# Performance work log

Measured on AMD Instinct MI355X. Metric: run time of the kernel, lower is better.

Reference implementation:

```python
import jax, jax.numpy as jnp
import numpy as np

N_NODES = 50000


def _gcn_conv(x, W, b, src, dst, n):
    # GCNConv (PyG semantics): x' = D^-1/2 (A + I) D^-1/2 (x W) + b
    h = x @ W  # [N, out]
    loop = jnp.arange(n, dtype=src.dtype)
    s = jnp.concatenate([src, loop])  # self-loops appended
    d = jnp.concatenate([dst, loop])
    deg = jax.ops.segment_sum(jnp.ones_like(d, dtype=h.dtype), d, num_segments=n)
    dinv = jnp.where(deg > 0, jax.lax.rsqrt(deg), 0.0)
    norm = dinv[s] * dinv[d]  # [E+N]
    msgs = norm[:, None] * h[s]  # gather: [E+N, out]
    out = jax.ops.segment_sum(msgs, d, num_segments=n)  # scatter-add
    return out + b


def setup_inputs() -> dict:
    key = jax.random.key(0)
    ks = jax.random.split(key, 6)
    n, din, dh, dout, e = N_NODES, 64, 64, 16, 1600000
    x = jax.random.normal(ks[0], (n, din), dtype=jnp.float32)
    edge_index = jax.random.randint(ks[1], (2, e), 0, n, dtype=jnp.int64)
    W1 = jax.random.normal(ks[2], (din, dh), dtype=jnp.float32) / np.sqrt(din)
    b1 = jnp.zeros((dh,), dtype=jnp.float32)
    W2 = jax.random.normal(ks[3], (dh, dout), dtype=jnp.float32) / np.sqrt(dh)
    b2 = jnp.zeros((dout,), dtype=jnp.float32)
    return {"x": x, "edge_index": edge_index, "W1": W1, "b1": b1, "W2": W2, "b2": b2}


def reference(x, edge_index, W1, b1, W2, b2):
    n = x.shape[0]
    src, dst = edge_index[0], edge_index[1]
    h = _gcn_conv(x, W1, b1, src, dst, n)
    h = jax.nn.relu(h)
    h = _gcn_conv(h, W2, b2, src, dst, n)
    return jax.nn.log_softmax(h, axis=1)
```

## Files before the change

### kernel.cpp

```cpp
#include <hip/hip_runtime.h>
#include <hip/hip_bf16.h>
#include <math.h>

#define BSHIFT 6
#define BNODES 64
#define MAXB 1024
#define SORTCAP 4096

__device__ __forceinline__ bool detect_f64(const void* edges, long long nn) {
    const long long* e64 = (const long long*)edges;
    bool ok = true;
#pragma unroll
    for (int i = 0; i < 8; ++i) {
        long long v = e64[i];
        ok = ok && (v >= 0 && v < nn);
    }
    return ok;
}

__device__ __forceinline__ float bf16lo(unsigned int u) {
    return __uint_as_float(u << 16);
}
__device__ __forceinline__ float bf16hi(unsigned int u) {
    return __uint_as_float(u & 0xFFFF0000u);
}
__device__ __forceinline__ float bf16dec(unsigned short u) {
    return __uint_as_float(((unsigned int)u) << 16);
}
__device__ __forceinline__ unsigned short bf16enc(float f) {
    __hip_bfloat16 h = __float2bfloat16(f);
    return *reinterpret_cast<unsigned short*>(&h);
}

__global__ __launch_bounds__(512) void k_hist(const void* edges, long long nn,
                                              long long E, long long epb,
                                              int nbuckets, int nblk, int* partial) {
    __shared__ int cnt[MAXB];
    int t = threadIdx.x;
    int i = blockIdx.x;
    for (int b = t; b < nbuckets; b += 512) cnt[b] = 0;
    __syncthreads();
    bool f64 = detect_f64(edges, nn);
    long long e0 = (long long)i * epb;
    long long e1 = e0 + epb; if (e1 > E) e1 = E;
    for (long long e = e0 + t; e < e1; e += 512) {
        int d = f64 ? (int)((const long long*)edges)[E + e] : ((const int*)edges)[E + e];
        atomicAdd(&cnt[d >> BSHIFT], 1);
    }
    __syncthreads();
    for (int b = t; b < nbuckets; b += 512) partial[b * nblk + i] = cnt[b];
}

__global__ __launch_bounds__(256) void k_scanB(int* partial, int nblk, int* totals) {
    __shared__ int tmp[256];
    int b = blockIdx.x, t = threadIdx.x;
    int v = (t < nblk) ? partial[b * nblk + t] : 0;
    tmp[t] = v;
    __syncthreads();
    for (int off = 1; off < 256; off <<= 1) {
        int a = (t >= off) ? tmp[t - off] : 0;
        __syncthreads();
        tmp[t] += a;
        __syncthreads();
    }
    if (t < nblk) partial[b * nblk + t] = tmp[t] - v;
    if (t == 255) totals[b] = tmp[255];
}

__global__ __launch_bounds__(1024) void k_scan(const int* __restrict__ totals, int nbuckets,
                                               int* base) {
    __shared__ int tmp[MAXB];
    int t = threadIdx.x;
    int v = (t < nbuckets) ? totals[t] : 0;
    tmp[t] = v;
    __syncthreads();
    for (int off = 1; off < MAXB; off <<= 1) {
        int a = (t >= off) ? tmp[t - off] : 0;
        __syncthreads();
        tmp[t] += a;
        __syncthreads();
    }
    if (t < nbuckets) base[t] = tmp[t] - v;
}

__global__ __launch_bounds__(512) void k_place(const void* edges, long long nn,
                                               long long E, long long epb,
                                               int nbuckets, int nblk,
                                               const int* __restrict__ base,
                                               const int* __restrict__ partial,
                                               unsigned int* keys) {
    __shared__ int cur[MAXB];
    int t = threadIdx.x;
    int i = blockIdx.x;
    for (int b = t; b < nbuckets; b += 512) cur[b] = base[b] + partial[b * nblk + i];
    __syncthreads();
    bool f64 = detect_f64(edges, nn);
    long long e0 = (long long)i * epb;
    long long e1 = e0 + epb; if (e1 > E) e1 = E;
    for (long long e = e0 + t; e < e1; e += 512) {
        int s, d;
        if (f64) {
            const long long* ee = (const long long*)edges;
            s = (int)ee[e]; d = (int)ee[E + e];
        } else {
            const int* ee = (const int*)edges;
            s = ee[e]; d = ee[E + e];
        }
        int pos = atomicAdd(&cur[d >> BSHIFT], 1);
        keys[pos] = (unsigned int)s | ((unsigned int)(d & (BNODES - 1)) << 17);
    }
}

__global__ __launch_bounds__(256) void k_sortdeg(unsigned int* keys,
                                                 const int* __restrict__ base,
                                                 const int* __restrict__ totals,
                                                 int* rowstart, int* counts,
                                                 float* dinv, int n,
                                                 unsigned int* scratch) {
    __shared__ unsigned int kbuf[SORTCAP];
    __shared__ int hist[BNODES];
    __shared__ int cur[BNODES];
    int t = threadIdx.x;
    int bk = blockIdx.x;
    int st = base[bk], c = totals[bk];
    if (t < BNODES) hist[t] = 0;
    __syncthreads();
    bool fits = (c <= SORTCAP);
    if (fits) {
        for (int i = t; i < c; i += 256) {
            unsigned int k = keys[st + i];
            kbuf[i] = k;
            atomicAdd(&hist[k >> 17], 1);
        }
    } else {
        for (int i = t; i < c; i += 256) {
            unsigned int k = keys[st + i];
            scratch[st + i] = k;
            atomicAdd(&hist[k >> 17], 1);
        }
    }
    __syncthreads();
    if (t < 64) {
        int v = hist[t];
        int incl = v;
        for (int o = 1; o < 64; o <<= 1) {
            int other = __shfl_up(incl, o, 64);
            if (t >= o) incl += other;
        }
        int ex = incl - v;
        cur[t] = ex;
        int node = bk * BNODES + t;
        if (node < n) {
            rowstart[node] = st + ex;
            counts[node] = v;
            dinv[node] = rsqrtf((float)v + 1.0f);
        }
    }
    __syncthreads();
    if (fits) {
        for (int i = t; i < c; i += 256) {
            unsigned int k = kbuf[i];
            int pos = atomicAdd(&cur[k >> 17], 1);
            keys[st + pos] = k & 0x1FFFFu;
        }
    } else {
        for (int i = t; i < c; i += 256) {
            unsigned int k = scratch[st + i];
            int pos = atomicAdd(&cur[k >> 17], 1);
            keys[st + pos] = k & 0x1FFFFu;
        }
    }
}

__global__ __launch_bounds__(256) void k_gemm1(const float* __restrict__ x,
                                               const float* __restrict__ W,
                                               const float* __restrict__ dinv,
                                               unsigned short* __restrict__ h) {
    __shared__ float Ws[64][64];
    __shared__ float xs[16][64];
    int t = threadIdx.x;
    for (int i = t; i < 64 * 64; i += 256) Ws[i >> 6][i & 63] = W[i];
    long long row0 = (long long)blockIdx.x * 16;
    ((float4*)xs)[t] = ((const float4*)(x + row0 * 64))[t];
    __syncthreads();
    int r = t >> 4, c0 = (t & 15) * 4;
    float4 acc = {0.f, 0.f, 0.f, 0.f};
#pragma unroll
    for (int k = 0; k < 64; ++k) {
        float xv = xs[r][k];
        float4 wv = *((const float4*)&Ws[k][c0]);
        acc.x += xv * wv.x; acc.y += xv * wv.y;
        acc.z += xv * wv.z; acc.w += xv * wv.w;
    }
    float di = dinv[row0 + r];
    ushort4 pk;
    pk.x = bf16enc(di * acc.x);
    pk.y = bf16enc(di * acc.y);
    pk.z = bf16enc(di * acc.z);
    pk.w = bf16enc(di * acc.w);
    *((ushort4*)(h + (row0 + r) * 64 + c0)) = pk;
}

__global__ __launch_bounds__(256) void k_gemm2(const unsigned short* __restrict__ h,
                                               const float* __restrict__ W,
                                               const float* __restrict__ dinv,
                                               unsigned short* __restrict__ h2) {
    __shared__ float Ws[64 * 16];
    __shared__ float xs[16][64];
    int t = threadIdx.x;
    for (int i = t; i < 64 * 16; i += 256) Ws[i] = W[i];
    long long row0 = (long long)blockIdx.x * 16;
    ushort4 u4 = ((const ushort4*)(h + row0 * 64))[t];
    int lr = t >> 4, lc = (t & 15) * 4;
    xs[lr][lc + 0] = bf16dec(u4.x);
    xs[lr][lc + 1] = bf16dec(u4.y);
    xs[lr][lc + 2] = bf16dec(u4.z);
    xs[lr][lc + 3] = bf16dec(u4.w);
    __syncthreads();
    int r = t >> 4, c = t & 15;
    float acc = 0.f;
#pragma unroll
    for (int k = 0; k < 64; ++k) acc += xs[r][k] * Ws[k * 16 + c];
    h2[(row0 + r) * 16 + c] = bf16enc(dinv[row0 + r] * acc);
}

__global__ __launch_bounds__(256) void k_agg64(const int* __restrict__ rowstart,
                                               const int* __restrict__ counts,
                                               const unsigned int* __restrict__ srcs,
                                               const unsigned int* __restrict__ hb2,
                                               const float* __restrict__ dinv,
                                               const float* __restrict__ b,
                                               unsigned short* __restrict__ out, int n) {
    int d = (blockIdx.x * 256 + threadIdx.x) >> 6;
    if (d >= n) return;
    int lane = threadIdx.x & 63;
    int half = lane >> 5;
    int fl = lane & 31;
    float ax = 0.f, ay = 0.f;
    if (half == 0) {
        unsigned int u = hb2[(long long)d * 32 + fl];
        ax = bf16lo(u); ay = bf16hi(u);
    }
    int start = rowstart[d];
    int cnt = counts[d];
    int k = 0;
    for (; k + 8 <= cnt; k += 8) {
        unsigned int s0 = srcs[start + k + half];
        unsigned int s1 = srcs[start + k + 2 + half];
        unsigned int s2 = srcs[start + k + 4 + half];
        unsigned int s3 = srcs[start + k + 6 + half];
        unsigned int u0 = hb2[(long long)s0 * 32 + fl];
        unsigned int u1 = hb2[(long long)s1 * 32 + fl];
        unsigned int u2 = hb2[(long long)s2 * 32 + fl];
        unsigned int u3 = hb2[(long long)s3 * 32 + fl];
        ax += bf16lo(u0); ay += bf16hi(u0);
        ax += bf16lo(u1); ay += bf16hi(u1);
        ax += bf16lo(u2); ay += bf16hi(u2);
        ax += bf16lo(u3); ay += bf16hi(u3);
    }
    for (; k < cnt; k += 2) {
        int idx = k + half;
        unsigned int u0 = 0;
        if (idx < cnt) u0 = hb2[(long long)srcs[start + idx] * 32 + fl];
        ax += bf16lo(u0); ay += bf16hi(u0);
    }
    ax += __shfl_xor(ax, 32);
    ay += __shfl_xor(ay, 32);
    float di = dinv[d];
    float2 bb = ((const float2*)b)[fl];
    float ox = fmaxf(di * ax + bb.x, 0.f);
    float oy = fmaxf(di * ay + bb.y, 0.f);
    if (half == 0) {
        unsigned int pk = (unsigned int)bf16enc(ox) | ((unsigned int)bf16enc(oy) << 16);
        ((unsigned int*)(out + (long long)d * 64))[fl] = pk;
    }
}

__global__ __launch_bounds__(256) void k_agg16(const int* __restrict__ rowstart,
                                               const int* __restrict__ counts,
                                               const unsigned int* __restrict__ srcs,
                                               const unsigned short* __restrict__ hb,
                                               const float* __restrict__ dinv,
                                               const float* __restrict__ b,
                                               float* __restrict__ out, int n) {
    int g = (blockIdx.x * 256 + threadIdx.x) >> 4;
    if (g >= n) return;
    int f = threadIdx.x & 15;
    long long rb = (long long)g * 16;
    float acc = bf16dec(hb[rb + f]);
    int start = rowstart[g];
    int cnt = counts[g];
    int k = 0;
    for (; k + 8 <= cnt; k += 8) {
        unsigned int s0 = srcs[start + k];
        unsigned int s1 = srcs[start + k + 1];
        unsigned int s2 = srcs[start + k + 2];
        unsigned int s3 = srcs[start + k + 3];
        unsigned int s4 = srcs[start + k + 4];
        unsigned int s5 = srcs[start + k + 5];
        unsigned int s6 = srcs[start + k + 6];
        unsigned int s7 = srcs[start + k + 7];
        unsigned short u0 = hb[(long long)s0 * 16 + f];
        unsigned short u1 = hb[(long long)s1 * 16 + f];
        unsigned short u2 = hb[(long long)s2 * 16 + f];
        unsigned short u3 = hb[(long long)s3 * 16 + f];
        unsigned short u4 = hb[(long long)s4 * 16 + f];
        unsigned short u5 = hb[(long long)s5 * 16 + f];
        unsigned short u6 = hb[(long long)s6 * 16 + f];
        unsigned short u7 = hb[(long long)s7 * 16 + f];
        acc += bf16dec(u0); acc += bf16dec(u1); acc += bf16dec(u2); acc += bf16dec(u3);
        acc += bf16dec(u4); acc += bf16dec(u5); acc += bf16dec(u6); acc += bf16dec(u7);
    }
    for (; k < cnt; ++k) acc += bf16dec(hb[(long long)srcs[start + k] * 16 + f]);
    float v = dinv[g] * acc + b[f];
    float m = v;
#pragma unroll
    for (int o = 8; o >= 1; o >>= 1) m = fmaxf(m, __shfl_xor(m, o, 16));
    float ex = __expf(v - m);
#pragma unroll
    for (int o = 8; o >= 1; o >>= 1) ex += __shfl_xor(ex, o, 16);
    out[rb + f] = (v - m) - __logf(ex);
}

extern "C" void kernel_launch(void* const* d_in, const int* in_sizes, int n_in,
                              void* d_out, int out_size, void* d_ws, size_t ws_size,
                              hipStream_t stream) {
    const float* x  = (const float*)d_in[0];
    const void*  ei = d_in[1];
    const float* W1 = (const float*)d_in[2];
    const float* b1 = (const float*)d_in[3];
    const float* W2 = (const float*)d_in[4];
    const float* b2 = (const float*)d_in[5];

    long long dh  = in_sizes[3];
    long long din = in_sizes[2] / dh;
    long long n   = in_sizes[0] / din;
    long long E   = (long long)in_sizes[1] / 2;
    int nbuckets  = (int)((n + BNODES - 1) >> BSHIFT);

    long long epb = 8192;
    while ((E + epb - 1) / epb > 256) epb <<= 1;
    int nblk = (int)((E + epb - 1) / epb);

    char* ws = (char*)d_ws;
    auto alloc = [&](size_t bytes) { void* p = ws; ws += (bytes + 255) & ~255ULL; return p; };
    int*   totals   = (int*)alloc(nbuckets * 4);
    int*   base     = (int*)alloc(nbuckets * 4);
    int*   rowstart = (int*)alloc(n * 4);
    int*   counts   = (int*)alloc(n * 4);
    float* dinv     = (float*)alloc(n * 4);
    int*   partial  = (int*)alloc((size_t)nbuckets * nblk * 4);
    unsigned int* keys = (unsigned int*)alloc(E * 4);
    unsigned short* h1b  = (unsigned short*)alloc(n * 64 * 2);
    unsigned short* out1 = (unsigned short*)alloc(n * 64 * 2);
    unsigned short* h2b  = (unsigned short*)alloc(n * 16 * 2);
    unsigned int* sort_scratch = (unsigned int*)out1;

    float* out = (float*)d_out;

    k_hist<<<nblk, 512, 0, stream>>>(ei, n, E, epb, nbuckets, nblk, partial);
    k_scanB<<<nbuckets, 256, 0, stream>>>(partial, nblk, totals);
    k_scan<<<1, 1024, 0, stream>>>(totals, nbuckets, base);
    k_place<<<nblk, 512, 0, stream>>>(ei, n, E, epb, nbuckets, nblk, base, partial, keys);
    k_sortdeg<<<nbuckets, 256, 0, stream>>>(keys, base, totals, rowstart, counts,
                                            dinv, (int)n, sort_scratch);

    k_gemm1<<<(int)(n / 16), 256, 0, stream>>>(x, W1, dinv, h1b);
    k_agg64<<<(int)((n * 64 + 255) / 256), 256, 0, stream>>>(
        rowstart, counts, keys, (const unsigned int*)h1b, dinv, b1, out1, (int)n);

    k_gemm2<<<(int)(n / 16), 256, 0, stream>>>(out1, W2, dinv, h2b);
    k_agg16<<<(int)((n * 16 + 255) / 256), 256, 0, stream>>>(
        rowstart, counts, keys, h2b, dinv, b2, out, (int)n);
}
```

Before: 123.7 us.

## Vectorize aggregation gathers and fuse global bucket scan into last scanB block

The aggregation kernels now have each lane load 16-byte (layer 1) or 8-byte (layer 2) chunks of a neighbor's bf16 row, so several edges are processed in parallel per wavefront and then reduced with shuffles. The log-softmax epilogue works on four values per lane. The separate single-block bucket scan kernel is removed: the last k_scanB block, chosen by an atomic ticket, scans the totals, at the cost of a memset and a threadfence. This aims to cut the number of memory transactions per gather and one kernel launch, in exchange for more shuffle reductions.

```diff
diff --git a/kernel.cpp b/kernel.cpp
--- a/kernel.cpp
+++ b/kernel.cpp
@@ -51,8 +51,10 @@
     for (int b = t; b < nbuckets; b += 512) partial[b * nblk + i] = cnt[b];
 }
 
-__global__ __launch_bounds__(256) void k_scanB(int* partial, int nblk, int* totals) {
+__global__ __launch_bounds__(256) void k_scanB(int* partial, int nblk, int nbuckets,
+                                               int* totals, int* base, int* ticket) {
     __shared__ int tmp[256];
+    __shared__ int lastflag;
     int b = blockIdx.x, t = threadIdx.x;
     int v = (t < nblk) ? partial[b * nblk + t] : 0;
     tmp[t] = v;
@@ -64,23 +66,34 @@
         __syncthreads();
     }
     if (t < nblk) partial[b * nblk + t] = tmp[t] - v;
-    if (t == 255) totals[b] = tmp[255];
-}
-
-__global__ __launch_bounds__(1024) void k_scan(const int* __restrict__ totals, int nbuckets,
-                                               int* base) {
-    __shared__ int tmp[MAXB];
-    int t = threadIdx.x;
-    int v = (t < nbuckets) ? totals[t] : 0;
-    tmp[t] = v;
-    __syncthreads();
-    for (int off = 1; off < MAXB; off <<= 1) {
+    if (t == 255) {
+        totals[b] = tmp[255];
+        __threadfence();
+        int r = atomicAdd(ticket, 1);
+        lastflag = (r == (int)gridDim.x - 1);
+    }
+    __syncthreads();
+    if (!lastflag) return;
+    int i0 = t * 4;
+    int x0 = (i0 + 0 < nbuckets) ? atomicAdd(&totals[i0 + 0], 0) : 0;
+    int x1 = (i0 + 1 < nbuckets) ? atomicAdd(&totals[i0 + 1], 0) : 0;
+    int x2 = (i0 + 2 < nbuckets) ? atomicAdd(&totals[i0 + 2], 0) : 0;
+    int x3 = (i0 + 3 < nbuckets) ? atomicAdd(&totals[i0 + 3], 0) : 0;
+    int s4 = x0 + x1 + x2 + x3;
+    __syncthreads();
+    tmp[t] = s4;
+    __syncthreads();
+    for (int off = 1; off < 256; off <<= 1) {
         int a = (t >= off) ? tmp[t - off] : 0;
         __syncthreads();
         tmp[t] += a;
         __syncthreads();
     }
-    if (t < nbuckets) base[t] = tmp[t] - v;
+    int ex = tmp[t] - s4;
+    if (i0 + 0 < nbuckets) base[i0 + 0] = ex;
+    if (i0 + 1 < nbuckets) base[i0 + 1] = ex + x0;
+    if (i0 + 2 < nbuckets) base[i0 + 2] = ex + x0 + x1;
+    if (i0 + 3 < nbuckets) base[i0 + 3] = ex + x0 + x1 + x2;
 }
 
 __global__ __launch_bounds__(512) void k_place(const void* edges, long long nn,
@@ -224,102 +237,140 @@
     h2[(row0 + r) * 16 + c] = bf16enc(dinv[row0 + r] * acc);
 }
 
+#define ACC8(u) do { \
+    a0 += bf16lo((u).x); a1 += bf16hi((u).x); \
+    a2 += bf16lo((u).y); a3 += bf16hi((u).y); \
+    a4 += bf16lo((u).z); a5 += bf16hi((u).z); \
+    a6 += bf16lo((u).w); a7 += bf16hi((u).w); } while (0)
+
 __global__ __launch_bounds__(256) void k_agg64(const int* __restrict__ rowstart,
                                                const int* __restrict__ counts,
                                                const unsigned int* __restrict__ srcs,
-                                               const unsigned int* __restrict__ hb2,
+                                               const uint4* __restrict__ hb8,
                                                const float* __restrict__ dinv,
                                                const float* __restrict__ b,
                                                unsigned short* __restrict__ out, int n) {
     int d = (blockIdx.x * 256 + threadIdx.x) >> 6;
     if (d >= n) return;
     int lane = threadIdx.x & 63;
-    int half = lane >> 5;
-    int fl = lane & 31;
-    float ax = 0.f, ay = 0.f;
-    if (half == 0) {
-        unsigned int u = hb2[(long long)d * 32 + fl];
-        ax = bf16lo(u); ay = bf16hi(u);
+    int g8 = lane >> 3;
+    int fq = lane & 7;
+    float a0 = 0.f, a1 = 0.f, a2 = 0.f, a3 = 0.f;
+    float a4 = 0.f, a5 = 0.f, a6 = 0.f, a7 = 0.f;
+    if (g8 == 0) {
+        uint4 u = hb8[(long long)d * 8 + fq];
+        ACC8(u);
     }
     int start = rowstart[d];
     int cnt = counts[d];
     int k = 0;
+    for (; k + 16 <= cnt; k += 16) {
+        unsigned int s0 = srcs[start + k + g8];
+        unsigned int s1 = srcs[start + k + 8 + g8];
+        uint4 u0 = hb8[(long long)s0 * 8 + fq];
+        uint4 u1 = hb8[(long long)s1 * 8 + fq];
+        ACC8(u0);
+        ACC8(u1);
+    }
     for (; k + 8 <= cnt; k += 8) {
-        unsigned int s0 = srcs[start + k + half];
-        unsigned int s1 = srcs[start + k + 2 + half];
-        unsigned int s2 = srcs[start + k + 4 + half];
-        unsigned int s3 = srcs[start + k + 6 + half];
-        unsigned int u0 = hb2[(long long)s0 * 32 + fl];
-        unsigned int u1 = hb2[(long long)s1 * 32 + fl];
-        unsigned int u2 = hb2[(long long)s2 * 32 + fl];
-        unsigned int u3 = hb2[(long long)s3 * 32 + fl];
-        ax += bf16lo(u0); ay += bf16hi(u0);
-        ax += bf16lo(u1); ay += bf16hi(u1);
-        ax += bf16lo(u2); ay += bf16hi(u2);
-        ax += bf16lo(u3); ay += bf16hi(u3);
-    }
-    for (; k < cnt; k += 2) {
-        int idx = k + half;
-        unsigned int u0 = 0;
-        if (idx < cnt) u0 = hb2[(long long)srcs[start + idx] * 32 + fl];
-        ax += bf16lo(u0); ay += bf16hi(u0);
-    }
-    ax += __shfl_xor(ax, 32);
-    ay += __shfl_xor(ay, 32);
-    float di = dinv[d];
-    float2 bb = ((const float2*)b)[fl];
-    float ox = fmaxf(di * ax + bb.x, 0.f);
-    float oy = fmaxf(di * ay + bb.y, 0.f);
-    if (half == 0) {
-        unsigned int pk = (unsigned int)bf16enc(ox) | ((unsigned int)bf16enc(oy) << 16);
-        ((unsigned int*)(out + (long long)d * 64))[fl] = pk;
+        unsigned int s0 = srcs[start + k + g8];
+        uint4 u0 = hb8[(long long)s0 * 8 + fq];
+        ACC8(u0);
+    }
+    if (k + g8 < cnt) {
+        unsigned int s0 = srcs[start + k + g8];
+        uint4 u0 = hb8[(long long)s0 * 8 + fq];
+        ACC8(u0);
+    }
+    a0 += __shfl_xor(a0, 8); a0 += __shfl_xor(a0, 16); a0 += __shfl_xor(a0, 32);
+    a1 += __shfl_xor(a1, 8); a1 += __shfl_xor(a1, 16); a1 += __shfl_xor(a1, 32);
+    a2 += __shfl_xor(a2, 8); a2 += __shfl_xor(a2, 16); a2 += __shfl_xor(a2, 32);
+    a3 += __shfl_xor(a3, 8); a3 += __shfl_xor(a3, 16); a3 += __shfl_xor(a3, 32);
+    a4 += __shfl_xor(a4, 8); a4 += __shfl_xor(a4, 16); a4 += __shfl_xor(a4, 32);
+    a5 += __shfl_xor(a5, 8); a5 += __shfl_xor(a5, 16); a5 += __shfl_xor(a5, 32);
+    a6 += __shfl_xor(a6, 8); a6 += __shfl_xor(a6, 16); a6 += __shfl_xor(a6, 32);
+    a7 += __shfl_xor(a7, 8); a7 += __shfl_xor(a7, 16); a7 += __shfl_xor(a7, 32);
+    if (g8 == 0) {
+        float di = dinv[d];
+        float4 b0 = ((const float4*)b)[2 * fq];
+        float4 b1 = ((const float4*)b)[2 * fq + 1];
+        float o0 = fmaxf(di * a0 + b0.x, 0.f);
+        float o1 = fmaxf(di * a1 + b0.y, 0.f);
+        float o2 = fmaxf(di * a2 + b0.z, 0.f);
+        float o3 = fmaxf(di * a3 + b0.w, 0.f);
+        float o4 = fmaxf(di * a4 + b1.x, 0.f);
+        float o5 = fmaxf(di * a5 + b1.y, 0.f);
+        float o6 = fmaxf(di * a6 + b1.z, 0.f);
+        float o7 = fmaxf(di * a7 + b1.w, 0.f);
+        uint4 pk;
+        pk.x = (unsigned int)bf16enc(o0) | ((unsigned int)bf16enc(o1) << 16);
+        pk.y = (unsigned int)bf16enc(o2) | ((unsigned int)bf16enc(o3) << 16);
+        pk.z = (unsigned int)bf16enc(o4) | ((unsigned int)bf16enc(o5) << 16);
+        pk.w = (unsigned int)bf16enc(o6) | ((unsigned int)bf16enc(o7) << 16);
+        ((uint4*)(out + (long long)d * 64))[fq] = pk;
     }
 }
 
 __global__ __launch_bounds__(256) void k_agg16(const int* __restrict__ rowstart,
                                                const int* __restrict__ counts,
                                                const unsigned int* __restrict__ srcs,
-                                               const unsigned short* __restrict__ hb,
+                                               const uint2* __restrict__ hb4,
                                                const float* __restrict__ dinv,
                                                const float* __restrict__ b,
                                                float* __restrict__ out, int n) {
     int g = (blockIdx.x * 256 + threadIdx.x) >> 4;
     if (g >= n) return;
-    int f = threadIdx.x & 15;
-    long long rb = (long long)g * 16;
-    float acc = bf16dec(hb[rb + f]);
+    int lane = threadIdx.x & 15;
+    int eg = lane >> 2;
+    int fp = lane & 3;
+    float a0 = 0.f, a1 = 0.f, a2 = 0.f, a3 = 0.f;
+    if (eg == 0) {
+        uint2 u = hb4[(long long)g * 4 + fp];
+        a0 = bf16lo(u.x); a1 = bf16hi(u.x); a2 = bf16lo(u.y); a3 = bf16hi(u.y);
+    }
     int start = rowstart[g];
     int cnt = counts[g];
     int k = 0;
     for (; k + 8 <= cnt; k += 8) {
-        unsigned int s0 = srcs[start + k];
-        unsigned int s1 = srcs[start + k + 1];
-        unsigned int s2 = srcs[start + k + 2];
-        unsigned int s3 = srcs[start + k + 3];
-        unsigned int s4 = srcs[start + k + 4];
-        unsigned int s5 = srcs[start + k + 5];
-        unsigned int s6 = srcs[start + k + 6];
-        unsigned int s7 = srcs[start + k + 7];
-        unsigned short u0 = hb[(long long)s0 * 16 + f];
-        unsigned short u1 = hb[(long long)s1 * 16 + f];
-        unsigned short u2 = hb[(long long)s2 * 16 + f];
-        unsigned short u3 = hb[(long long)s3 * 16 + f];
-        unsigned short u4 = hb[(long long)s4 * 16 + f];
-        unsigned short u5 = hb[(long long)s5 * 16 + f];
-        unsigned short u6 = hb[(long long)s6 * 16 + f];
-        unsigned short u7 = hb[(long long)s7 * 16 + f];
-        acc += bf16dec(u0); acc += bf16dec(u1); acc += bf16dec(u2); acc += bf16dec(u3);
-        acc += bf16dec(u4); acc += bf16dec(u5); acc += bf16dec(u6); acc += bf16dec(u7);
-    }
-    for (; k < cnt; ++k) acc += bf16dec(hb[(long long)srcs[start + k] * 16 + f]);
-    float v = dinv[g] * acc + b[f];
-    float m = v;
-#pragma unroll
-    for (int o = 8; o >= 1; o >>= 1) m = fmaxf(m, __shfl_xor(m, o, 16));
-    float ex = __expf(v - m);
-#pragma unroll
-    for (int o = 8; o >= 1; o >>= 1) ex += __shfl_xor(ex, o, 16);
-    out[rb + f] = (v - m) - __logf(ex);
+        unsigned int s0 = srcs[start + k + eg];
+        unsigned int s1 = srcs[start + k + 4 + eg];
+        uint2 u0 = hb4[(long long)s0 * 4 + fp];
+        uint2 u1 = hb4[(long long)s1 * 4 + fp];
+        a0 += bf16lo(u0.x); a1 += bf16hi(u0.x); a2 += bf16lo(u0.y); a3 += bf16hi(u0.y);
+        a0 += bf16lo(u1.x); a1 += bf16hi(u1.x); a2 += bf16lo(u1.y); a3 += bf16hi(u1.y);
+    }
+    for (; k + 4 <= cnt; k += 4) {
+        unsigned int s0 = srcs[start + k + eg];
+        uint2 u0 = hb4[(long long)s0 * 4 + fp];
+        a0 += bf16lo(u0.x); a1 += bf16hi(u0.x); a2 += bf16lo(u0.y); a3 += bf16hi(u0.y);
+    }
+    if (k + eg < cnt) {
+        unsigned int s0 = srcs[start + k + eg];
+        uint2 u0 = hb4[(long long)s0 * 4 + fp];
+        a0 += bf16lo(u0.x); a1 += bf16hi(u0.x); a2 += bf16lo(u0.y); a3 += bf16hi(u0.y);
+    }
+    a0 += __shfl_xor(a0, 4); a0 += __shfl_xor(a0, 8);
+    a1 += __shfl_xor(a1, 4); a1 += __shfl_xor(a1, 8);
+    a2 += __shfl_xor(a2, 4); a2 += __shfl_xor(a2, 8);
+    a3 += __shfl_xor(a3, 4); a3 += __shfl_xor(a3, 8);
+    float di = dinv[g];
+    float4 bb = ((const float4*)b)[fp];
+    float v0 = di * a0 + bb.x;
+    float v1 = di * a1 + bb.y;
+    float v2 = di * a2 + bb.z;
+    float v3 = di * a3 + bb.w;
+    float m = fmaxf(fmaxf(v0, v1), fmaxf(v2, v3));
+    m = fmaxf(m, __shfl_xor(m, 1));
+    m = fmaxf(m, __shfl_xor(m, 2));
+    float ex = __expf(v0 - m) + __expf(v1 - m) + __expf(v2 - m) + __expf(v3 - m);
+    ex += __shfl_xor(ex, 1);
+    ex += __shfl_xor(ex, 2);
+    float lse = __logf(ex) + m;
+    if (eg == 0) {
+        float4 o4;
+        o4.x = v0 - lse; o4.y = v1 - lse; o4.z = v2 - lse; o4.w = v3 - lse;
+        ((float4*)(out + (long long)g * 16))[fp] = o4;
+    }
 }
 
 extern "C" void kernel_launch(void* const* d_in, const int* in_sizes, int n_in,
@@ -344,6 +395,7 @@
 
     char* ws = (char*)d_ws;
     auto alloc = [&](size_t bytes) { void* p = ws; ws += (bytes + 255) & ~255ULL; return p; };
+    int*   ticket   = (int*)alloc(4);
     int*   totals   = (int*)alloc(nbuckets * 4);
     int*   base     = (int*)alloc(nbuckets * 4);
     int*   rowstart = (int*)alloc(n * 4);
@@ -358,18 +410,19 @@
 
     float* out = (float*)d_out;
 
+    hipMemsetAsync(ticket, 0, 4, stream);
+
     k_hist<<<nblk, 512, 0, stream>>>(ei, n, E, epb, nbuckets, nblk, partial);
-    k_scanB<<<nbuckets, 256, 0, stream>>>(partial, nblk, totals);
-    k_scan<<<1, 1024, 0, stream>>>(totals, nbuckets, base);
+    k_scanB<<<nbuckets, 256, 0, stream>>>(partial, nblk, nbuckets, totals, base, ticket);
     k_place<<<nblk, 512, 0, stream>>>(ei, n, E, epb, nbuckets, nblk, base, partial, keys);
     k_sortdeg<<<nbuckets, 256, 0, stream>>>(keys, base, totals, rowstart, counts,
                                             dinv, (int)n, sort_scratch);
 
     k_gemm1<<<(int)(n / 16), 256, 0, stream>>>(x, W1, dinv, h1b);
     k_agg64<<<(int)((n * 64 + 255) / 256), 256, 0, stream>>>(
-        rowstart, counts, keys, (const unsigned int*)h1b, dinv, b1, out1, (int)n);
+        rowstart, counts, keys, (const uint4*)h1b, dinv, b1, out1, (int)n);
 
     k_gemm2<<<(int)(n / 16), 256, 0, stream>>>(out1, W2, dinv, h2b);
     k_agg16<<<(int)((n * 16 + 255) / 256), 256, 0, stream>>>(
-        rowstart, counts, keys, h2b, dinv, b2, out, (int)n);
-}
+        rowstart, counts, keys, (const uint2*)h2b, dinv, b2, out, (int)n);
+}
```

Measured after the change: 133.8 us. 1.08x slower.
